# Kernel tuning notes

Hardware: AMD Instinct MI355X
Metric: run time of the kernel (lower is better)

The kernel has to match this reference:

```python
import jax, jax.numpy as jnp
import numpy as np

N_HEAD = 12
HEAD_DIM = 64
N_EMBD = 768
ATTN_MULT = 0.125
B, T = 2, 2048
NEG_INF = -1e30


def setup_inputs() -> dict:
    key = jax.random.key(0)
    ks = jax.random.split(key, 3)
    x = jax.random.normal(ks[0], (B, T, N_EMBD), dtype=jnp.float32)
    W_attn = jax.random.normal(ks[1], (N_EMBD, 3 * N_HEAD * HEAD_DIM), dtype=jnp.float32) * 0.02
    b_attn = jnp.zeros((3 * N_HEAD * HEAD_DIM,), dtype=jnp.float32)
    W_proj = jax.random.normal(ks[2], (N_HEAD * HEAD_DIM, N_EMBD), dtype=jnp.float32) * 0.02
    b_proj = jnp.zeros((N_EMBD,), dtype=jnp.float32)
    return {"x": x, "W_attn": W_attn, "b_attn": b_attn, "W_proj": W_proj, "b_proj": b_proj}


def reference(x, W_attn, b_attn, W_proj, b_proj):
    Bsz, Tlen, C = x.shape
    H, D = N_HEAD, HEAD_DIM
    qkv = x @ W_attn + b_attn                       # [B,T,3*H*D]
    q, k, v = jnp.split(qkv, 3, axis=-1)
    q = q.reshape(Bsz, Tlen, H, D).transpose(0, 2, 1, 3)   # [B,H,T,D]
    k = k.reshape(Bsz, Tlen, H, D).transpose(0, 2, 1, 3)
    v = v.reshape(Bsz, Tlen, H, D).transpose(0, 2, 1, 3)

    att = jnp.einsum('bhtd,bhsd->bhts', q, k) * ATTN_MULT  # [B,H,T,T]
    causal = jnp.tril(jnp.ones((Tlen, Tlen), dtype=bool))  # [T,T]
    att = jnp.where(causal, att, NEG_INF)

    # selection mask from head 0 (SelectionHeadLinearComboKind.NONE)
    S = jax.nn.relu(att[:, 0:1, :, :])                     # [B,1,T,T]; relu kills -inf
    # protect_bos_token: zero column 0 (key index 0)
    col = jnp.arange(Tlen)
    S = S * (col[None, None, None, :] != 0)
    # prevent_from_masking_myself: zero diagonal
    S = S * (1.0 - jnp.eye(Tlen, dtype=S.dtype))

    # accumulate selection over query (row) axis: ProtectionKind.NONE
    FF = jnp.cumsum(S, axis=-2)                            # [B,1,T,T]
    att = att - FF                                         # broadcast over heads

    p = jax.nn.softmax(att, axis=-1)                       # [B,H,T,T]
    y = jnp.einsum('bhts,bhsd->bhtd', p, v)                # [B,H,T,D]
    y = y.transpose(0, 2, 1, 3).reshape(Bsz, Tlen, H * D)  # [B,T,H*D]
    return y @ W_proj + b_proj
```

## Files before the change

### kernel.cpp

```cpp
#include <hip/hip_runtime.h>
#include <math.h>

#define T 2048
#define NH 12
#define HD 64
#define C3 2304
#define CE 768
#define NB 2

typedef __attribute__((ext_vector_type(8))) short bf16x8;
typedef __attribute__((ext_vector_type(4))) float f32x4;
typedef __attribute__((ext_vector_type(16))) float f32x16;
typedef __attribute__((ext_vector_type(4))) unsigned u32x4;

__device__ inline void bf16split(float a, unsigned short& h, unsigned short& l) {
    unsigned int u = __float_as_uint(a);
    unsigned int r = (u + 0x7FFFu + ((u >> 16) & 1u)) >> 16;
    h = (unsigned short)r;
    float hf = __uint_as_float(r << 16);
    float lo = a - hf;
    unsigned int v = __float_as_uint(lo);
    l = (unsigned short)((v + 0x7FFFu + ((v >> 16) & 1u)) >> 16);
}

__device__ inline void packP(float a, float b, unsigned& wh, unsigned& wl) {
    unsigned short ha, la, hb, lb;
    bf16split(a, ha, la); bf16split(b, hb, lb);
    wh = (unsigned)ha | ((unsigned)hb << 16);
    wl = (unsigned)la | ((unsigned)lb << 16);
}

__global__ __launch_bounds__(256) void cvt_split_kernel(const float* __restrict__ A,
        unsigned short* __restrict__ H, unsigned short* __restrict__ L) {
    int i = blockIdx.x * 256 + threadIdx.x;
    float4 a0 = *(reinterpret_cast<const float4*>(A) + (size_t)i * 2);
    float4 a1 = *(reinterpret_cast<const float4*>(A) + (size_t)i * 2 + 1);
    float f[8] = {a0.x, a0.y, a0.z, a0.w, a1.x, a1.y, a1.z, a1.w};
    unsigned short h[8], l[8];
    #pragma unroll
    for (int j = 0; j < 8; ++j) bf16split(f[j], h[j], l[j]);
    uint4 hv, lv;
    hv.x = (unsigned)h[0] | ((unsigned)h[1] << 16); hv.y = (unsigned)h[2] | ((unsigned)h[3] << 16);
    hv.z = (unsigned)h[4] | ((unsigned)h[5] << 16); hv.w = (unsigned)h[6] | ((unsigned)h[7] << 16);
    lv.x = (unsigned)l[0] | ((unsigned)l[1] << 16); lv.y = (unsigned)l[2] | ((unsigned)l[3] << 16);
    lv.z = (unsigned)l[4] | ((unsigned)l[5] << 16); lv.w = (unsigned)l[6] | ((unsigned)l[7] << 16);
    reinterpret_cast<uint4*>(H)[i] = hv;
    reinterpret_cast<uint4*>(L)[i] = lv;
}

__global__ __launch_bounds__(256) void cvt_split_T_kernel(const float* __restrict__ W,
        unsigned short* __restrict__ H, unsigned short* __restrict__ L, int K, int N) {
    __shared__ float tile[64][65];
    const int n0 = blockIdx.x * 64, k0 = blockIdx.y * 64;
    const int t = threadIdx.x;
    {
        int r = t >> 2, c4 = (t & 3) * 16;
        #pragma unroll
        for (int u = 0; u < 4; ++u) {
            float4 w = *reinterpret_cast<const float4*>(&W[(size_t)(k0 + r) * N + n0 + c4 + u * 4]);
            tile[r][c4 + u * 4 + 0] = w.x; tile[r][c4 + u * 4 + 1] = w.y;
            tile[r][c4 + u * 4 + 2] = w.z; tile[r][c4 + u * 4 + 3] = w.w;
        }
    }
    __syncthreads();
    {
        int n = t >> 2, kc = (t & 3) * 16;
        unsigned short h[16], l[16];
        #pragma unroll
        for (int j = 0; j < 16; ++j) bf16split(tile[kc + j][n], h[j], l[j]);
        uint4 hv0, hv1, lv0, lv1;
        hv0.x = (unsigned)h[0] | ((unsigned)h[1] << 16);  hv0.y = (unsigned)h[2] | ((unsigned)h[3] << 16);
        hv0.z = (unsigned)h[4] | ((unsigned)h[5] << 16);  hv0.w = (unsigned)h[6] | ((unsigned)h[7] << 16);
        hv1.x = (unsigned)h[8] | ((unsigned)h[9] << 16);  hv1.y = (unsigned)h[10] | ((unsigned)h[11] << 16);
        hv1.z = (unsigned)h[12] | ((unsigned)h[13] << 16); hv1.w = (unsigned)h[14] | ((unsigned)h[15] << 16);
        lv0.x = (unsigned)l[0] | ((unsigned)l[1] << 16);  lv0.y = (unsigned)l[2] | ((unsigned)l[3] << 16);
        lv0.z = (unsigned)l[4] | ((unsigned)l[5] << 16);  lv0.w = (unsigned)l[6] | ((unsigned)l[7] << 16);
        lv1.x = (unsigned)l[8] | ((unsigned)l[9] << 16);  lv1.y = (unsigned)l[10] | ((unsigned)l[11] << 16);
        lv1.z = (unsigned)l[12] | ((unsigned)l[13] << 16); lv1.w = (unsigned)l[14] | ((unsigned)l[15] << 16);
        size_t o = (size_t)(n0 + n) * K + k0 + kc;
        reinterpret_cast<uint4*>(&H[o])[0] = hv0; reinterpret_cast<uint4*>(&H[o])[1] = hv1;
        reinterpret_cast<uint4*>(&L[o])[0] = lv0; reinterpret_cast<uint4*>(&L[o])[1] = lv1;
    }
}

__global__ __launch_bounds__(256) void cvt_kv_vt_kernel(const float* __restrict__ Vtmp,
        unsigned short* __restrict__ Vh, unsigned short* __restrict__ Vl) {
    __shared__ float tile[64][65];
    const int s0 = blockIdx.x * 64;
    const int bh = blockIdx.y;
    const int tid = threadIdx.x;
    {
        int r = tid >> 2, c0 = (tid & 3) * 16;
        const float* src = Vtmp + ((size_t)bh * T + s0 + r) * 64 + c0;
        #pragma unroll
        for (int u = 0; u < 4; ++u) {
            float4 w = *reinterpret_cast<const float4*>(src + u * 4);
            tile[r][c0 + u * 4 + 0] = w.x; tile[r][c0 + u * 4 + 1] = w.y;
            tile[r][c0 + u * 4 + 2] = w.z; tile[r][c0 + u * 4 + 3] = w.w;
        }
    }
    __syncthreads();
    {
        int d = tid >> 2, cs = (tid & 3) * 16;
        unsigned short hh[16], ll[16];
        #pragma unroll
        for (int j = 0; j < 16; ++j) bf16split(tile[cs + j][d], hh[j], ll[j]);
        uint4 hv0, hv1, lv0, lv1;
        hv0.x = (unsigned)hh[0] | ((unsigned)hh[1] << 16);  hv0.y = (unsigned)hh[2] | ((unsigned)hh[3] << 16);
        hv0.z = (unsigned)hh[4] | ((unsigned)hh[5] << 16);  hv0.w = (unsigned)hh[6] | ((unsigned)hh[7] << 16);
        hv1.x = (unsigned)hh[8] | ((unsigned)hh[9] << 16);  hv1.y = (unsigned)hh[10] | ((unsigned)hh[11] << 16);
        hv1.z = (unsigned)hh[12] | ((unsigned)hh[13] << 16); hv1.w = (unsigned)hh[14] | ((unsigned)hh[15] << 16);
        lv0.x = (unsigned)ll[0] | ((unsigned)ll[1] << 16);  lv0.y = (unsigned)ll[2] | ((unsigned)ll[3] << 16);
        lv0.z = (unsigned)ll[4] | ((unsigned)ll[5] << 16);  lv0.w = (unsigned)ll[6] | ((unsigned)ll[7] << 16);
        lv1.x = (unsigned)ll[8] | ((unsigned)ll[9] << 16);  lv1.y = (unsigned)ll[10] | ((unsigned)ll[11] << 16);
        lv1.z = (unsigned)ll[12] | ((unsigned)ll[13] << 16); lv1.w = (unsigned)ll[14] | ((unsigned)ll[15] << 16);
        size_t o = ((size_t)bh * 64 + d) * T + s0 + cs;
        reinterpret_cast<uint4*>(&Vh[o])[0] = hv0; reinterpret_cast<uint4*>(&Vh[o])[1] = hv1;
        reinterpret_cast<uint4*>(&Vl[o])[0] = lv0; reinterpret_cast<uint4*>(&Vl[o])[1] = lv1;
    }
}

#define LDST 40
__global__ __launch_bounds__(256) void gemm_mfma_kernel(
        const unsigned short* __restrict__ Ah, const unsigned short* __restrict__ Al,
        const unsigned short* __restrict__ Bh, const unsigned short* __restrict__ Bl,
        const float* __restrict__ bias, float* __restrict__ Cm,
        int M, int N, int K) {
    __shared__ unsigned short lA[2][128 * LDST];
    __shared__ unsigned short lB[2][128 * LDST];
    const int tid = threadIdx.x;
    const int bm = blockIdx.y * 128, bn = blockIdx.x * 128;
    const int lane = tid & 63, wid = tid >> 6;
    const int wr = wid >> 1, wc = wid & 1;
    f32x4 acc[4][4];
    #pragma unroll
    for (int i = 0; i < 4; ++i)
        #pragma unroll
        for (int j = 0; j < 4; ++j) acc[i][j] = (f32x4){0.f, 0.f, 0.f, 0.f};
    const int srow = tid >> 2, sk8 = (tid & 3) * 8;
    const int arb = wr * 64 + (lane & 15);
    const int brb = wc * 64 + (lane & 15);
    const int koff = (lane >> 4) * 8;
    for (int k0 = 0; k0 < K; k0 += 32) {
        __syncthreads();
        #pragma unroll
        for (int c = 0; c < 2; ++c) {
            int row = srow + 64 * c;
            uint4 va = *reinterpret_cast<const uint4*>(&Ah[(size_t)(bm + row) * K + k0 + sk8]);
            uint4 vb = *reinterpret_cast<const uint4*>(&Al[(size_t)(bm + row) * K + k0 + sk8]);
            uint4 vc = *reinterpret_cast<const uint4*>(&Bh[(size_t)(bn + row) * K + k0 + sk8]);
            uint4 vd = *reinterpret_cast<const uint4*>(&Bl[(size_t)(bn + row) * K + k0 + sk8]);
            *reinterpret_cast<uint4*>(&lA[0][row * LDST + sk8]) = va;
            *reinterpret_cast<uint4*>(&lA[1][row * LDST + sk8]) = vb;
            *reinterpret_cast<uint4*>(&lB[0][row * LDST + sk8]) = vc;
            *reinterpret_cast<uint4*>(&lB[1][row * LDST + sk8]) = vd;
        }
        __syncthreads();
        bf16x8 fa[2][4], fb[2][4];
        #pragma unroll
        for (int fi = 0; fi < 4; ++fi) {
            fa[0][fi] = *reinterpret_cast<const bf16x8*>(&lA[0][(arb + fi * 16) * LDST + koff]);
            fa[1][fi] = *reinterpret_cast<const bf16x8*>(&lA[1][(arb + fi * 16) * LDST + koff]);
            fb[0][fi] = *reinterpret_cast<const bf16x8*>(&lB[0][(brb + fi * 16) * LDST + koff]);
            fb[1][fi] = *reinterpret_cast<const bf16x8*>(&lB[1][(brb + fi * 16) * LDST + koff]);
        }
        #pragma unroll
        for (int fi = 0; fi < 4; ++fi)
            #pragma unroll
            for (int fj = 0; fj < 4; ++fj) {
                acc[fi][fj] = __builtin_amdgcn_mfma_f32_16x16x32_bf16(fb[0][fj], fa[0][fi], acc[fi][fj], 0, 0, 0);
                acc[fi][fj] = __builtin_amdgcn_mfma_f32_16x16x32_bf16(fb[0][fj], fa[1][fi], acc[fi][fj], 0, 0, 0);
                acc[fi][fj] = __builtin_amdgcn_mfma_f32_16x16x32_bf16(fb[1][fj], fa[0][fi], acc[fi][fj], 0, 0, 0);
            }
    }
    const int mloc = lane & 15, ng = (lane >> 4) * 4;
    #pragma unroll
    for (int fi = 0; fi < 4; ++fi) {
        int row = bm + wr * 64 + fi * 16 + mloc;
        #pragma unroll
        for (int fj = 0; fj < 4; ++fj) {
            int n0 = bn + wc * 64 + fj * 16 + ng;
            float4 bv = *reinterpret_cast<const float4*>(&bias[n0]);
            float4 o4 = {acc[fi][fj][0] + bv.x, acc[fi][fj][1] + bv.y,
                         acc[fi][fj][2] + bv.z, acc[fi][fj][3] + bv.w};
            *reinterpret_cast<float4*>(&Cm[(size_t)row * N + n0]) = o4;
        }
    }
}

__global__ __launch_bounds__(256) void gemm_qkv_mfma_kernel(
        const unsigned short* __restrict__ Ah, const unsigned short* __restrict__ Al,
        const unsigned short* __restrict__ Bh, const unsigned short* __restrict__ Bl,
        const float* __restrict__ bias,
        unsigned short* __restrict__ Qh, unsigned short* __restrict__ Ql,
        unsigned short* __restrict__ Kh, unsigned short* __restrict__ Kl,
        float* __restrict__ Vtmp) {
    const int K = CE;
    __shared__ unsigned short lA[2][128 * LDST];
    __shared__ unsigned short lB[2][128 * LDST];
    const int tid = threadIdx.x;
    const int bm = blockIdx.y * 128, bn = blockIdx.x * 128;
    const int lane = tid & 63, wid = tid >> 6;
    const int wr = wid >> 1, wc = wid & 1;
    f32x4 acc[4][4];
    #pragma unroll
    for (int i = 0; i < 4; ++i)
        #pragma unroll
        for (int j = 0; j < 4; ++j) acc[i][j] = (f32x4){0.f, 0.f, 0.f, 0.f};
    const int srow = tid >> 2, sk8 = (tid & 3) * 8;
    const int arb = wr * 64 + (lane & 15);
    const int brb = wc * 64 + (lane & 15);
    const int koff = (lane >> 4) * 8;
    for (int k0 = 0; k0 < K; k0 += 32) {
        __syncthreads();
        #pragma unroll
        for (int c = 0; c < 2; ++c) {
            int row = srow + 64 * c;
            uint4 va = *reinterpret_cast<const uint4*>(&Ah[(size_t)(bm + row) * K + k0 + sk8]);
            uint4 vb = *reinterpret_cast<const uint4*>(&Al[(size_t)(bm + row) * K + k0 + sk8]);
            uint4 vc = *reinterpret_cast<const uint4*>(&Bh[(size_t)(bn + row) * K + k0 + sk8]);
            uint4 vd = *reinterpret_cast<const uint4*>(&Bl[(size_t)(bn + row) * K + k0 + sk8]);
            *reinterpret_cast<uint4*>(&lA[0][row * LDST + sk8]) = va;
            *reinterpret_cast<uint4*>(&lA[1][row * LDST + sk8]) = vb;
            *reinterpret_cast<uint4*>(&lB[0][row * LDST + sk8]) = vc;
            *reinterpret_cast<uint4*>(&lB[1][row * LDST + sk8]) = vd;
        }
        __syncthreads();
        bf16x8 fa[2][4], fb[2][4];
        #pragma unroll
        for (int fi = 0; fi < 4; ++fi) {
            fa[0][fi] = *reinterpret_cast<const bf16x8*>(&lA[0][(arb + fi * 16) * LDST + koff]);
            fa[1][fi] = *reinterpret_cast<const bf16x8*>(&lA[1][(arb + fi * 16) * LDST + koff]);
            fb[0][fi] = *reinterpret_cast<const bf16x8*>(&lB[0][(brb + fi * 16) * LDST + koff]);
            fb[1][fi] = *reinterpret_cast<const bf16x8*>(&lB[1][(brb + fi * 16) * LDST + koff]);
        }
        #pragma unroll
        for (int fi = 0; fi < 4; ++fi)
            #pragma unroll
            for (int fj = 0; fj < 4; ++fj) {
                acc[fi][fj] = __builtin_amdgcn_mfma_f32_16x16x32_bf16(fb[0][fj], fa[0][fi], acc[fi][fj], 0, 0, 0);
                acc[fi][fj] = __builtin_amdgcn_mfma_f32_16x16x32_bf16(fb[0][fj], fa[1][fi], acc[fi][fj], 0, 0, 0);
                acc[fi][fj] = __builtin_amdgcn_mfma_f32_16x16x32_bf16(fb[1][fj], fa[0][fi], acc[fi][fj], 0, 0, 0);
            }
    }
    const int colbase = bn + wc * 64;
    const int region = colbase / 768;
    const int h = (colbase % 768) >> 6;
    const int mloc = lane & 15, ng = (lane >> 4) * 4;
    #pragma unroll
    for (int fi = 0; fi < 4; ++fi) {
        int tg = bm + wr * 64 + fi * 16 + mloc;
        int bb = tg >> 11, t = tg & (T - 1);
        #pragma unroll
        for (int fj = 0; fj < 4; ++fj) {
            int dbase = fj * 16 + ng;
            float4 bv = *reinterpret_cast<const float4*>(&bias[colbase + dbase]);
            float v0 = acc[fi][fj][0] + bv.x, v1 = acc[fi][fj][1] + bv.y;
            float v2 = acc[fi][fj][2] + bv.z, v3 = acc[fi][fj][3] + bv.w;
            size_t o = ((size_t)(bb * NH + h) * T + t) * 64 + dbase;
            if (region == 2) {
                float4 o4 = {v0, v1, v2, v3};
                *reinterpret_cast<float4*>(&Vtmp[o]) = o4;
            } else {
                unsigned short hh[4], ll[4];
                bf16split(v0, hh[0], ll[0]); bf16split(v1, hh[1], ll[1]);
                bf16split(v2, hh[2], ll[2]); bf16split(v3, hh[3], ll[3]);
                uint2 ph = {(unsigned)hh[0] | ((unsigned)hh[1] << 16),
                            (unsigned)hh[2] | ((unsigned)hh[3] << 16)};
                uint2 pl = {(unsigned)ll[0] | ((unsigned)ll[1] << 16),
                            (unsigned)ll[2] | ((unsigned)ll[3] << 16)};
                if (region == 0) {
                    *reinterpret_cast<uint2*>(&Qh[o]) = ph;
                    *reinterpret_cast<uint2*>(&Ql[o]) = pl;
                } else {
                    *reinterpret_cast<uint2*>(&Kh[o]) = ph;
                    *reinterpret_cast<uint2*>(&Kl[o]) = pl;
                }
            }
        }
    }
}

__global__ __launch_bounds__(256) void gemm_bias_kernel(
        const float* __restrict__ A, const float* __restrict__ B,
        const float* __restrict__ bias, float* __restrict__ Cm,
        int M, int N, int K) {
    __shared__ float As[16][64];
    __shared__ float Bs[16][68];
    const int tid = threadIdx.x;
    const int ty = tid >> 4, tx = tid & 15;
    const int bm = blockIdx.y * 64, bn = blockIdx.x * 64;
    float acc[4][4] = {};
    for (int k0 = 0; k0 < K; k0 += 16) {
        {
            int r = tid >> 2;
            int kk = (tid & 3) * 4;
            float4 a = *reinterpret_cast<const float4*>(&A[(size_t)(bm + r) * K + k0 + kk]);
            As[kk + 0][r] = a.x; As[kk + 1][r] = a.y; As[kk + 2][r] = a.z; As[kk + 3][r] = a.w;
        }
        {
            int kk = tid >> 4;
            int c = (tid & 15) * 4;
            *reinterpret_cast<float4*>(&Bs[kk][c]) =
                *reinterpret_cast<const float4*>(&B[(size_t)(k0 + kk) * N + bn + c]);
        }
        __syncthreads();
        #pragma unroll
        for (int kk = 0; kk < 16; ++kk) {
            float4 a4 = *reinterpret_cast<const float4*>(&As[kk][ty * 4]);
            float4 b4 = *reinterpret_cast<const float4*>(&Bs[kk][tx * 4]);
            float av[4] = {a4.x, a4.y, a4.z, a4.w};
            float bv[4] = {b4.x, b4.y, b4.z, b4.w};
            #pragma unroll
            for (int i = 0; i < 4; ++i)
                #pragma unroll
                for (int j = 0; j < 4; ++j)
                    acc[i][j] = fmaf(av[i], bv[j], acc[i][j]);
        }
        __syncthreads();
    }
    #pragma unroll
    for (int i = 0; i < 4; ++i) {
        int row = bm + ty * 4 + i;
        #pragma unroll
        for (int j = 0; j < 4; ++j) {
            int col = bn + tx * 4 + j;
            Cm[(size_t)row * N + col] = acc[i][j] + bias[col];
        }
    }
}

#define FST 72

__global__ __launch_bounds__(256) void s0_mfma_kernel(
        const unsigned short* __restrict__ Qh, const unsigned short* __restrict__ Ql,
        const unsigned short* __restrict__ Kh, const unsigned short* __restrict__ Kl,
        float* __restrict__ S, float* __restrict__ Psum) {
    const int kb = blockIdx.x * 64, qb = blockIdx.y * 64, b = blockIdx.z;
    const int tid = threadIdx.x;
    float* Sb = S + (size_t)b * T * T;
    if (kb > qb) {
        const int ty = tid >> 4, tx = tid & 15;
        #pragma unroll
        for (int i = 0; i < 4; ++i) {
            float4 z = {0.f, 0.f, 0.f, 0.f};
            *reinterpret_cast<float4*>(&Sb[(size_t)(qb + ty * 4 + i) * T + kb + tx * 4]) = z;
        }
        if (tid < 64) Psum[((size_t)(b * 32 + (qb >> 6)) * T) + kb + tid] = 0.f;
        return;
    }
    const int lane = tid & 63, w = tid >> 6;
    const int fr = lane & 15, fg = lane >> 4;
    __shared__ unsigned short Ks[2][64 * FST];
    __shared__ float csum[4][64];
    const int hb0 = b * NH;
    {
        const int sr = tid >> 2, sc0 = (tid & 3) * 16;
        const unsigned short* kh = Kh + ((size_t)hb0 * T + kb + sr) * 64 + sc0;
        const unsigned short* kl = Kl + ((size_t)hb0 * T + kb + sr) * 64 + sc0;
        uint4 a0 = reinterpret_cast<const uint4*>(kh)[0];
        uint4 a1 = reinterpret_cast<const uint4*>(kh)[1];
        uint4 b0 = reinterpret_cast<const uint4*>(kl)[0];
        uint4 b1 = reinterpret_cast<const uint4*>(kl)[1];
        *reinterpret_cast<uint4*>(&Ks[0][sr * FST + sc0 + 0]) = a0;
        *reinterpret_cast<uint4*>(&Ks[0][sr * FST + sc0 + 8]) = a1;
        *reinterpret_cast<uint4*>(&Ks[1][sr * FST + sc0 + 0]) = b0;
        *reinterpret_cast<uint4*>(&Ks[1][sr * FST + sc0 + 8]) = b1;
    }
    bf16x8 qh[2], ql[2];
    #pragma unroll
    for (int ks = 0; ks < 2; ++ks) {
        size_t qo = ((size_t)hb0 * T + qb + w * 16 + fr) * 64 + ks * 32 + fg * 8;
        qh[ks] = *reinterpret_cast<const bf16x8*>(&Qh[qo]);
        ql[ks] = *reinterpret_cast<const bf16x8*>(&Ql[qo]);
    }
    __syncthreads();
    f32x4 qk[4];
    #pragma unroll
    for (int fj = 0; fj < 4; ++fj) qk[fj] = (f32x4){0.f, 0.f, 0.f, 0.f};
    #pragma unroll
    for (int ks = 0; ks < 2; ++ks) {
        bf16x8 kbh[4], kbl[4];
        #pragma unroll
        for (int fj = 0; fj < 4; ++fj) {
            kbh[fj] = *reinterpret_cast<const bf16x8*>(&Ks[0][(fj * 16 + fr) * FST + ks * 32 + fg * 8]);
            kbl[fj] = *reinterpret_cast<const bf16x8*>(&Ks[1][(fj * 16 + fr) * FST + ks * 32 + fg * 8]);
        }
        #pragma unroll
        for (int fj = 0; fj < 4; ++fj) {
            qk[fj] = __builtin_amdgcn_mfma_f32_16x16x32_bf16(qh[ks], kbh[fj], qk[fj], 0, 0, 0);
            qk[fj] = __builtin_amdgcn_mfma_f32_16x16x32_bf16(qh[ks], kbl[fj], qk[fj], 0, 0, 0);
            qk[fj] = __builtin_amdgcn_mfma_f32_16x16x32_bf16(ql[ks], kbh[fj], qk[fj], 0, 0, 0);
        }
    }
    float colsum[4] = {0.f, 0.f, 0.f, 0.f};
    #pragma unroll
    for (int p = 0; p < 4; ++p) {
        int t = qb + w * 16 + fg * 4 + p;
        #pragma unroll
        for (int fj = 0; fj < 4; ++fj) {
            int s = kb + fj * 16 + fr;
            float v = qk[fj][p] * 0.125f;
            float o = (s >= 1 && s < t) ? fmaxf(v, 0.0f) : 0.0f;
            Sb[(size_t)t * T + s] = o;
            colsum[fj] += o;
        }
    }
    #pragma unroll
    for (int fj = 0; fj < 4; ++fj) {
        colsum[fj] += __shfl_xor(colsum[fj], 16);
        colsum[fj] += __shfl_xor(colsum[fj], 32);
    }
    if (lane < 16) {
        #pragma unroll
        for (int fj = 0; fj < 4; ++fj) csum[w][fj * 16 + lane] = colsum[fj];
    }
    __syncthreads();
    if (tid < 64) {
        float v = csum[0][tid] + csum[1][tid] + csum[2][tid] + csum[3][tid];
        Psum[((size_t)(b * 32 + (qb >> 6)) * T) + kb + tid] = v;
    }
}

__global__ __launch_bounds__(256) void s0_kernel(const float* __restrict__ qkv,
                                                 float* __restrict__ S) {
    const int kb = blockIdx.x * 64, qb = blockIdx.y * 64, b = blockIdx.z;
    const int tid = threadIdx.x, ty = tid >> 4, tx = tid & 15;
    float* Sb = S + (size_t)b * T * T;
    if (kb > qb) {
        #pragma unroll
        for (int i = 0; i < 4; ++i) {
            int row = qb + ty * 4 + i;
            float4 z = {0.f, 0.f, 0.f, 0.f};
            *reinterpret_cast<float4*>(&Sb[(size_t)row * T + kb + tx * 4]) = z;
        }
        return;
    }
    __shared__ float Qt[64][68];
    __shared__ float Kt[64][68];
    {
        int r = tid >> 2;
        int c0 = (tid & 3) * 16;
        const float* qrow = qkv + (size_t)(b * T + qb + r) * C3 + 0;
        const float* krow = qkv + (size_t)(b * T + kb + r) * C3 + 768;
        #pragma unroll
        for (int u = 0; u < 4; ++u) {
            float4 q4 = *reinterpret_cast<const float4*>(&qrow[c0 + u * 4]);
            float4 k4 = *reinterpret_cast<const float4*>(&krow[c0 + u * 4]);
            int d = c0 + u * 4;
            Qt[d + 0][r] = q4.x; Qt[d + 1][r] = q4.y; Qt[d + 2][r] = q4.z; Qt[d + 3][r] = q4.w;
            Kt[d + 0][r] = k4.x; Kt[d + 1][r] = k4.y; Kt[d + 2][r] = k4.z; Kt[d + 3][r] = k4.w;
        }
    }
    __syncthreads();
    float acc[4][4] = {};
    #pragma unroll
    for (int d = 0; d < 64; ++d) {
        float4 qv = *reinterpret_cast<const float4*>(&Qt[d][ty * 4]);
        float4 kv = *reinterpret_cast<const float4*>(&Kt[d][tx * 4]);
        float qa[4] = {qv.x, qv.y, qv.z, qv.w};
        float ka[4] = {kv.x, kv.y, kv.z, kv.w};
        #pragma unroll
        for (int i = 0; i < 4; ++i)
            #pragma unroll
            for (int j = 0; j < 4; ++j)
                acc[i][j] = fmaf(qa[i], ka[j], acc[i][j]);
    }
    #pragma unroll
    for (int i = 0; i < 4; ++i) {
        int t = qb + ty * 4 + i;
        float o[4];
        #pragma unroll
        for (int j = 0; j < 4; ++j) {
            int s = kb + tx * 4 + j;
            float v = acc[i][j] * 0.125f;
            o[j] = (s >= 1 && s < t) ? fmaxf(v, 0.0f) : 0.0f;
        }
        float4 o4 = {o[0], o[1], o[2], o[3]};
        *reinterpret_cast<float4*>(&Sb[(size_t)t * T + kb + tx * 4]) = o4;
    }
}

__global__ __launch_bounds__(256) void colsum_kernel(const float* __restrict__ S,
                                                     float* __restrict__ Psum) {
    int s = blockIdx.x * 256 + threadIdx.x;
    int j = blockIdx.y, b = blockIdx.z;
    const float* Sb = S + (size_t)b * T * T;
    float sum = 0.f;
    for (int r = 0; r < 64; ++r) sum += Sb[(size_t)(j * 64 + r) * T + s];
    Psum[((size_t)b * 32 + j) * T + s] = sum;
}

__global__ __launch_bounds__(256) void scanseg_kernel(float* __restrict__ Psum) {
    int s = blockIdx.x * 256 + threadIdx.x;
    int b = blockIdx.y;
    float v[32];
    #pragma unroll
    for (int j = 0; j < 32; ++j)
        v[j] = Psum[((size_t)(b * 32 + j)) * T + s];
    float run = 0.f;
    #pragma unroll
    for (int j = 0; j < 32; ++j) {
        Psum[((size_t)(b * 32 + j)) * T + s] = run;
        run += v[j];
    }
}

__global__ __launch_bounds__(256) void ffscan_kernel(float* __restrict__ S,
                                                     const float* __restrict__ Psum) {
    int s = blockIdx.x * 256 + threadIdx.x;
    int j = blockIdx.y, b = blockIdx.z;
    float run = Psum[((size_t)b * 32 + j) * T + s];
    float* Sb = S + (size_t)b * T * T;
    for (int r = 0; r < 64; ++r) {
        size_t idx = (size_t)(j * 64 + r) * T + s;
        run += Sb[idx];
        Sb[idx] = run;
    }
}

__device__ const int FTQ[40] = {15,15,15,15,14,14,14,13,13,13,12,12,12,11,11,11,10,10,9,9,8,8,7,7,6,5,4,3,14,10,6,2,13,9,5,1,12,8,4,0};
__device__ const int FK0[40] = {0,8,16,24,0,8,16,0,8,16,0,8,16,0,8,16,0,8,0,8,0,8,0,8,0,0,0,0,24,16,8,0,24,16,8,0,24,16,8,0};
__device__ const int FK1[40] = {8,16,24,32,8,16,24,8,16,24,8,16,24,8,16,24,8,16,8,16,8,16,8,16,8,8,8,8,30,22,14,6,28,20,12,4,26,18,10,2};
__device__ const int FCB[12] = {0,2,4,6,8,11,14,17,20,24,28,32};

__global__ __launch_bounds__(256) void flash_mfma_kernel(
        const unsigned short* __restrict__ Qh, const unsigned short* __restrict__ Ql,
        const unsigned short* __restrict__ Kh, const unsigned short* __restrict__ Kl,
        const unsigned short* __restrict__ Vth, const unsigned short* __restrict__ Vtl,
        const float* __restrict__ FF,
        unsigned short* __restrict__ Yh, unsigned short* __restrict__ Yl,
        float* __restrict__ PART) {
    const int hb = blockIdx.x;
    const int h = hb % NH, b = hb / NH;
    const int u = blockIdx.y;
    const int tq = FTQ[u], kt0 = FK0[u], kt1 = FK1[u];
    const int qb = tq * 128;
// ... 519 lines not shown
```

Baseline: 250.5 us.

## Use direct global-to-LDS loads with XOR swizzle and block remap in GEMMs

```diff
diff --git a/kernel.cpp b/kernel.cpp
--- a/kernel.cpp
+++ b/kernel.cpp
@@ -12,6 +12,12 @@
 typedef __attribute__((ext_vector_type(4))) float f32x4;
 typedef __attribute__((ext_vector_type(16))) float f32x16;
 typedef __attribute__((ext_vector_type(4))) unsigned u32x4;
+
+__device__ __forceinline__ void gload16(const void* g, void* l) {
+    __builtin_amdgcn_global_load_lds(
+        (const __attribute__((address_space(1))) void*)g,
+        (__attribute__((address_space(3))) void*)l, 16, 0, 0);
+}
 
 __device__ inline void bf16split(float a, unsigned short& h, unsigned short& l) {
     unsigned int u = __float_as_uint(a);
@@ -120,16 +126,19 @@
     }
 }
 
-#define LDST 40
+#define LD32 32
 __global__ __launch_bounds__(256) void gemm_mfma_kernel(
         const unsigned short* __restrict__ Ah, const unsigned short* __restrict__ Al,
         const unsigned short* __restrict__ Bh, const unsigned short* __restrict__ Bl,
         const float* __restrict__ bias, float* __restrict__ Cm,
         int M, int N, int K) {
-    __shared__ unsigned short lA[2][128 * LDST];
-    __shared__ unsigned short lB[2][128 * LDST];
+    __shared__ unsigned short lA[2][128 * LD32];
+    __shared__ unsigned short lB[2][128 * LD32];
     const int tid = threadIdx.x;
-    const int bm = blockIdx.y * 128, bn = blockIdx.x * 128;
+    const int nwg = gridDim.x * gridDim.y;
+    int bid = blockIdx.y * gridDim.x + blockIdx.x;
+    bid = (bid & 7) * (nwg >> 3) + (bid >> 3);
+    const int bm = (bid / gridDim.x) * 128, bn = (bid % gridDim.x) * 128;
     const int lane = tid & 63, wid = tid >> 6;
     const int wr = wid >> 1, wc = wid & 1;
     f32x4 acc[4][4];
@@ -137,32 +146,39 @@
     for (int i = 0; i < 4; ++i)
         #pragma unroll
         for (int j = 0; j < 4; ++j) acc[i][j] = (f32x4){0.f, 0.f, 0.f, 0.f};
-    const int srow = tid >> 2, sk8 = (tid & 3) * 8;
+    const int srow0 = wid * 32 + (lane >> 2);
+    const int scn   = lane & 3;
     const int arb = wr * 64 + (lane & 15);
     const int brb = wc * 64 + (lane & 15);
-    const int koff = (lane >> 4) * 8;
+    const int kc  = lane >> 4;
     for (int k0 = 0; k0 < K; k0 += 32) {
         __syncthreads();
         #pragma unroll
-        for (int c = 0; c < 2; ++c) {
-            int row = srow + 64 * c;
-            uint4 va = *reinterpret_cast<const uint4*>(&Ah[(size_t)(bm + row) * K + k0 + sk8]);
-            uint4 vb = *reinterpret_cast<const uint4*>(&Al[(size_t)(bm + row) * K + k0 + sk8]);
-            uint4 vc = *reinterpret_cast<const uint4*>(&Bh[(size_t)(bn + row) * K + k0 + sk8]);
-            uint4 vd = *reinterpret_cast<const uint4*>(&Bl[(size_t)(bn + row) * K + k0 + sk8]);
-            *reinterpret_cast<uint4*>(&lA[0][row * LDST + sk8]) = va;
-            *reinterpret_cast<uint4*>(&lA[1][row * LDST + sk8]) = vb;
-            *reinterpret_cast<uint4*>(&lB[0][row * LDST + sk8]) = vc;
-            *reinterpret_cast<uint4*>(&lB[1][row * LDST + sk8]) = vd;
+        for (int h = 0; h < 2; ++h) {
+            int row = srow0 + h * 16;
+            int cs = scn ^ ((row >> 1) & 3);
+            size_t ao = (size_t)(bm + row) * K + k0 + cs * 8;
+            size_t bo = (size_t)(bn + row) * K + k0 + cs * 8;
+            unsigned short* d0 = &lA[0][(wid * 32 + h * 16) * LD32];
+            unsigned short* d1 = &lA[1][(wid * 32 + h * 16) * LD32];
+            unsigned short* d2 = &lB[0][(wid * 32 + h * 16) * LD32];
+            unsigned short* d3 = &lB[1][(wid * 32 + h * 16) * LD32];
+            gload16(&Ah[ao], d0);
+            gload16(&Al[ao], d1);
+            gload16(&Bh[bo], d2);
+            gload16(&Bl[bo], d3);
         }
         __syncthreads();
         bf16x8 fa[2][4], fb[2][4];
         #pragma unroll
         for (int fi = 0; fi < 4; ++fi) {
-            fa[0][fi] = *reinterpret_cast<const bf16x8*>(&lA[0][(arb + fi * 16) * LDST + koff]);
-            fa[1][fi] = *reinterpret_cast<const bf16x8*>(&lA[1][(arb + fi * 16) * LDST + koff]);
-            fb[0][fi] = *reinterpret_cast<const bf16x8*>(&lB[0][(brb + fi * 16) * LDST + koff]);
-            fb[1][fi] = *reinterpret_cast<const bf16x8*>(&lB[1][(brb + fi * 16) * LDST + koff]);
+            int ra = arb + fi * 16, rb = brb + fi * 16;
+            int ca = (kc ^ ((ra >> 1) & 3)) * 8;
+            int cb = (kc ^ ((rb >> 1) & 3)) * 8;
+            fa[0][fi] = *reinterpret_cast<const bf16x8*>(&lA[0][ra * LD32 + ca]);
+            fa[1][fi] = *reinterpret_cast<const bf16x8*>(&lA[1][ra * LD32 + ca]);
+            fb[0][fi] = *reinterpret_cast<const bf16x8*>(&lB[0][rb * LD32 + cb]);
+            fb[1][fi] = *reinterpret_cast<const bf16x8*>(&lB[1][rb * LD32 + cb]);
         }
         #pragma unroll
         for (int fi = 0; fi < 4; ++fi)
@@ -196,10 +212,13 @@
         unsigned short* __restrict__ Kh, unsigned short* __restrict__ Kl,
         float* __restrict__ Vtmp) {
     const int K = CE;
-    __shared__ unsigned short lA[2][128 * LDST];
-    __shared__ unsigned short lB[2][128 * LDST];
+    __shared__ unsigned short lA[2][128 * LD32];
+    __shared__ unsigned short lB[2][128 * LD32];
     const int tid = threadIdx.x;
-    const int bm = blockIdx.y * 128, bn = blockIdx.x * 128;
+    const int nwg = gridDim.x * gridDim.y;
+    int bid = blockIdx.y * gridDim.x + blockIdx.x;
+    bid = (bid & 7) * (nwg >> 3) + (bid >> 3);
+    const int bm = (bid / gridDim.x) * 128, bn = (bid % gridDim.x) * 128;
     const int lane = tid & 63, wid = tid >> 6;
     const int wr = wid >> 1, wc = wid & 1;
     f32x4 acc[4][4];
@@ -207,32 +226,39 @@
     for (int i = 0; i < 4; ++i)
         #pragma unroll
         for (int j = 0; j < 4; ++j) acc[i][j] = (f32x4){0.f, 0.f, 0.f, 0.f};
-    const int srow = tid >> 2, sk8 = (tid & 3) * 8;
+    const int srow0 = wid * 32 + (lane >> 2);
+    const int scn   = lane & 3;
     const int arb = wr * 64 + (lane & 15);
     const int brb = wc * 64 + (lane & 15);
-    const int koff = (lane >> 4) * 8;
+    const int kc  = lane >> 4;
     for (int k0 = 0; k0 < K; k0 += 32) {
         __syncthreads();
         #pragma unroll
-        for (int c = 0; c < 2; ++c) {
-            int row = srow + 64 * c;
-            uint4 va = *reinterpret_cast<const uint4*>(&Ah[(size_t)(bm + row) * K + k0 + sk8]);
-            uint4 vb = *reinterpret_cast<const uint4*>(&Al[(size_t)(bm + row) * K + k0 + sk8]);
-            uint4 vc = *reinterpret_cast<const uint4*>(&Bh[(size_t)(bn + row) * K + k0 + sk8]);
-            uint4 vd = *reinterpret_cast<const uint4*>(&Bl[(size_t)(bn + row) * K + k0 + sk8]);
-            *reinterpret_cast<uint4*>(&lA[0][row * LDST + sk8]) = va;
-            *reinterpret_cast<uint4*>(&lA[1][row * LDST + sk8]) = vb;
-            *reinterpret_cast<uint4*>(&lB[0][row * LDST + sk8]) = vc;
-            *reinterpret_cast<uint4*>(&lB[1][row * LDST + sk8]) = vd;
+        for (int h = 0; h < 2; ++h) {
+            int row = srow0 + h * 16;
+            int cs = scn ^ ((row >> 1) & 3);
+            size_t ao = (size_t)(bm + row) * K + k0 + cs * 8;
+            size_t bo = (size_t)(bn + row) * K + k0 + cs * 8;
+            unsigned short* d0 = &lA[0][(wid * 32 + h * 16) * LD32];
+            unsigned short* d1 = &lA[1][(wid * 32 + h * 16) * LD32];
+            unsigned short* d2 = &lB[0][(wid * 32 + h * 16) * LD32];
+            unsigned short* d3 = &lB[1][(wid * 32 + h * 16) * LD32];
+            gload16(&Ah[ao], d0);
+            gload16(&Al[ao], d1);
+            gload16(&Bh[bo], d2);
+            gload16(&Bl[bo], d3);
         }
         __syncthreads();
         bf16x8 fa[2][4], fb[2][4];
         #pragma unroll
         for (int fi = 0; fi < 4; ++fi) {
-            fa[0][fi] = *reinterpret_cast<const bf16x8*>(&lA[0][(arb + fi * 16) * LDST + koff]);
-            fa[1][fi] = *reinterpret_cast<const bf16x8*>(&lA[1][(arb + fi * 16) * LDST + koff]);
-            fb[0][fi] = *reinterpret_cast<const bf16x8*>(&lB[0][(brb + fi * 16) * LDST + koff]);
-            fb[1][fi] = *reinterpret_cast<const bf16x8*>(&lB[1][(brb + fi * 16) * LDST + koff]);
+            int ra = arb + fi * 16, rb = brb + fi * 16;
+            int ca = (kc ^ ((ra >> 1) & 3)) * 8;
+            int cb = (kc ^ ((rb >> 1) & 3)) * 8;
+            fa[0][fi] = *reinterpret_cast<const bf16x8*>(&lA[0][ra * LD32 + ca]);
+            fa[1][fi] = *reinterpret_cast<const bf16x8*>(&lA[1][ra * LD32 + ca]);
+            fb[0][fi] = *reinterpret_cast<const bf16x8*>(&lB[0][rb * LD32 + cb]);
+            fb[1][fi] = *reinterpret_cast<const bf16x8*>(&lB[1][rb * LD32 + cb]);
         }
         #pragma unroll
         for (int fi = 0; fi < 4; ++fi)
```

New measurement: 246.4 us. No clear change (-1.6%).
